# Kernel tuning notes

Measured on AMD Instinct MI355X. Metric: run time of the kernel, lower is better.

## Reference

```python
import jax, jax.numpy as jnp
import numpy as np

BLOCKS = (1, 2, 3, 4)      # (block_size, offset=0) from max_block_size=4
BLOCK_MULT = 12            # lcm(1,2,3,4)
DS = 4                     # downsample_factor
MAX_BS = 4                 # max block size (also pos_conv kernel size)
DIM = 512
VOCAB = 256


def _masked_mean(t, m, axis):
    # t: [..., L, D], m: [..., L] bool -> mean over axis with mask, 0 where empty
    mf = m[..., None].astype(t.dtype)
    num = jnp.sum(t * mf, axis=axis)
    tot = jnp.sum(mf, axis=axis)
    mean = num / jnp.clip(tot, 1.0)
    return jnp.where(tot == 0.0, jnp.zeros_like(mean), mean)


def setup_inputs() -> dict:
    key = jax.random.key(0)
    ks = jax.random.split(key, 8)
    B, S = 8, 2048
    return {
        "x": jax.random.randint(ks[0], (B, S), 0, VOCAB),
        "mask": jnp.ones((B, S), dtype=bool),
        "emb": jax.random.normal(ks[1], (VOCAB, DIM), jnp.float32) * 0.02,
        "dw_w": jax.random.normal(ks[2], (MAX_BS, 1, DIM), jnp.float32) * 0.1,   # depthwise kernel (W, I=1, O=DIM)
        "dw_b": jnp.zeros((DIM,), jnp.float32),
        "pw_w": jax.random.normal(ks[3], (1, DIM, DIM), jnp.float32) * 0.03,     # pointwise 1x1 conv
        "pw_b": jnp.zeros((DIM,), jnp.float32),
        "score_w": jax.random.normal(ks[4], (DIM, 1), jnp.float32) * 0.05,
        "score_b": jnp.zeros((1,), jnp.float32),
    }


def reference(x, mask, emb, dw_w, dw_b, pw_w, pw_b, score_w, score_b):
    B, S = x.shape
    D = DIM
    trunc = ((S + DS - 1) // DS) * DS  # next_divisible_length(S, DS); equals S here

    h = emb[x]                                              # [B,S,D]
    h = jnp.pad(h, ((0, 0), (0, MAX_BS - 1), (0, 0)))       # right pad for VALID conv
    dn = jax.lax.conv_dimension_numbers(h.shape, dw_w.shape, ('NWC', 'WIO', 'NWC'))
    h = jax.lax.conv_general_dilated(h, dw_w, (1,), 'VALID',
                                     dimension_numbers=dn,
                                     feature_group_count=D) + dw_b  # depthwise -> [B,S,D]
    h = jnp.einsum('bsd,de->bse', h, pw_w[0]) + pw_b                # pointwise

    # pad seq to multiple of lcm of block sizes
    Sp = ((h.shape[1] + BLOCK_MULT - 1) // BLOCK_MULT) * BLOCK_MULT
    pad = Sp - h.shape[1]
    h = jnp.pad(h, ((0, 0), (0, pad), (0, 0)))
    m = jnp.pad(mask.astype(bool), ((0, 0), (0, pad)), constant_values=False)

    reprs, rmasks = [], []
    for bsz in BLOCKS:  # fixed small set of block sizes (offset=0 for all)
        nb = Sp // bsz
        g = h.reshape(B, nb, bsz, D)
        mg = m.reshape(B, nb, bsz)
        r = _masked_mean(g, mg, axis=2)                       # [B,nb,D]
        reprs.append(jnp.repeat(r, bsz, axis=1))              # [B,Sp,D]
        rmasks.append(jnp.repeat(jnp.any(mg, axis=-1), bsz, axis=1))

    block_reprs = jnp.stack(reprs, axis=2)    # [B,Sp,M,D]
    block_masks = jnp.stack(rmasks, axis=2)   # [B,Sp,M]

    scores = (block_reprs @ score_w)[..., 0] + score_b[0]     # [B,Sp,M]
    max_neg = -jnp.finfo(scores.dtype).max
    scores = jnp.where(block_masks, scores, max_neg)
    scores = jnp.nan_to_num(jax.nn.softmax(scores, axis=2), nan=0.0)

    # consensus attention over positions
    sim = jnp.einsum('bim,bjm->bij', scores, scores)          # [B,Sp,Sp]
    cm = m[:, :, None] & m[:, None, :]
    sim = jnp.where(cm, sim, max_neg)
    attn = jnp.nan_to_num(jax.nn.softmax(sim, axis=-1), nan=0.0)
    scores = jnp.einsum('bij,bjm->bim', attn, scores)

    out = jnp.einsum('bsmd,bsm->bsd', block_reprs, scores)    # weighted combine
    out = out[:, :trunc]
    mt = m[:, :trunc]

    nl = trunc // DS
    xb = out.reshape(B, nl, DS, D)
    mb = mt.reshape(B, nl, DS)
    out = _masked_mean(xb, mb, axis=2)                        # [B, S/DS, D]
    out_mask = jnp.any(mb, axis=-1)
    return out, out_mask
```

## Files before the change

### kernel.cpp

```cpp
#include <hip/hip_runtime.h>
#include <stdint.h>
#include <stddef.h>

typedef __bf16 bf16_t;
typedef bf16_t bf16x4v __attribute__((ext_vector_type(4)));
typedef bf16_t bf16x8v __attribute__((ext_vector_type(8)));
typedef float  f32x4   __attribute__((ext_vector_type(4)));

#define NBATCH 8
#define SEQ    2048
#define DIM    512
#define SP     2052
#define NB2    1026
#define NB3    684
#define NB4    513
#define NL     512

static __device__ __forceinline__ f32x4 ldbf4(const bf16_t* p) {
  bf16x4v v = *(const bf16x4v*)p;
  f32x4 r;
  r.x = (float)v[0]; r.y = (float)v[1]; r.z = (float)v[2]; r.w = (float)v[3];
  return r;
}
static __device__ __forceinline__ void stbf4(bf16_t* p, f32x4 v) {
  bf16x4v o;
  o[0] = (bf16_t)v.x; o[1] = (bf16_t)v.y; o[2] = (bf16_t)v.z; o[3] = (bf16_t)v.w;
  *(bf16x4v*)p = o;
}

static __device__ __forceinline__ void gload_lds16(const void* g, void* l) {
  __builtin_amdgcn_global_load_lds(
      (const __attribute__((address_space(1))) void*)g,
      (__attribute__((address_space(3))) void*)l, 16, 0, 0);
}

#define GP_WT   256
#define GP_MASK 65
#define GP_AP   512
#define GP_B2   2
__global__ __launch_bounds__(256) void kPrep(
    const float* __restrict__ pw, bf16_t* __restrict__ Wt,
    const void* __restrict__ mraw, float* __restrict__ mask01,
    const float* __restrict__ emb, const float* __restrict__ dww,
    const float* __restrict__ dwb, const float* __restrict__ pwb,
    bf16_t* __restrict__ Ap, float* __restrict__ bias2) {
  const int bx = blockIdx.x, t = threadIdx.x;
  if (bx < GP_WT) {
    __shared__ float T[32][33];
    int ti = bx >> 4, tj = bx & 15;
    int r = t >> 3, c0 = (t & 7) * 4;
    f32x4 v = *(const f32x4*)(pw + (size_t)(ti * 32 + r) * DIM + tj * 32 + c0);
    T[c0 + 0][r] = v.x; T[c0 + 1][r] = v.y;
    T[c0 + 2][r] = v.z; T[c0 + 3][r] = v.w;
    __syncthreads();
    bf16x4v o;
    o[0] = (bf16_t)T[r][c0 + 0]; o[1] = (bf16_t)T[r][c0 + 1];
    o[2] = (bf16_t)T[r][c0 + 2]; o[3] = (bf16_t)T[r][c0 + 3];
    *(bf16x4v*)(Wt + (size_t)(tj * 32 + r) * DIM + ti * 32 + c0) = o;
    return;
  }
  if (bx < GP_WT + GP_MASK) {
    int idx = (bx - GP_WT) * 256 + t;
    if (idx >= NBATCH * SP) return;
    int b = idx / SP, s = idx - b * SP;
    const unsigned char* mb = (const unsigned char*)mraw;
    int u8 = 0;
#pragma unroll
    for (int i = 0; i < 64; i++)
      if ((i & 3) != 0 && mb[i] != 0) u8 = 1;
    float v = 0.f;
    if (s < SEQ) {
      int mi = b * SEQ + s;
      int nz = u8 ? (mb[mi] != 0) : (((const int*)mraw)[mi] != 0);
      v = nz ? 1.f : 0.f;
    }
    mask01[idx] = v;
    return;
  }
  if (bx < GP_WT + GP_MASK + GP_AP) {
    int rp = bx - (GP_WT + GP_MASK);
    int row = rp * 2 + (t >> 7);
    int v = row & 255, tt = row >> 8;
    int d0 = (t & 127) * 4;
    f32x4 e = *(const f32x4*)(emb + (size_t)v * DIM + d0);
    f32x4 w = *(const f32x4*)(dww + tt * DIM + d0);
    stbf4(Ap + (size_t)row * DIM + d0, e * w);
    return;
  }
  {
    int e = (bx - (GP_WT + GP_MASK + GP_AP)) * 256 + t;
    float acc = pwb[e];
#pragma unroll 8
    for (int d = 0; d < DIM; d++) acc += dwb[d] * pw[(size_t)d * DIM + e];
    bias2[e] = acc;
  }
}

#define BM 64
#define BN 128
#define BK 32
__global__ __launch_bounds__(256) void kG_gemm(
    const bf16_t* __restrict__ A, const bf16_t* __restrict__ Bt,
    bf16_t* __restrict__ G) {
  __shared__ __align__(16) bf16_t As[BM * BK];
  __shared__ __align__(16) bf16_t Bs[BN * BK];
  const int t = threadIdx.x;
  const int mt = blockIdx.x >> 2, nt = blockIdx.x & 3;
  const int m0 = mt * BM, n0 = nt * BN;
  const int lane = t & 63, wave = t >> 6;
  const int wm = (wave & 1) * 32, wn = (wave >> 1) * 64;
  const int mloc = lane & 15, quad = lane >> 4;

  f32x4 acc[2][4] = {};

  char* asd  = (char*)As + t * 16;
  char* bsd1 = (char*)Bs + t * 16;
  char* bsd2 = (char*)Bs + (t + 256) * 16;
  const int ar = t >> 2, ak = (t & 3) * 8;
  const int br2 = (t + 256) >> 2;

  for (int k0 = 0; k0 < 512; k0 += BK) {
    gload_lds16(A + (size_t)(m0 + ar) * DIM + k0 + ak, asd);
    gload_lds16(Bt + (size_t)(n0 + ar) * DIM + k0 + ak, bsd1);
    gload_lds16(Bt + (size_t)(n0 + br2) * DIM + k0 + ak, bsd2);
    __syncthreads();
    bf16x8v af[2], bfr[4];
#pragma unroll
    for (int i = 0; i < 2; i++)
      af[i] = *(const bf16x8v*)&As[(wm + i * 16 + mloc) * BK + quad * 8];
#pragma unroll
    for (int i = 0; i < 4; i++)
      bfr[i] = *(const bf16x8v*)&Bs[(wn + i * 16 + mloc) * BK + quad * 8];
#pragma unroll
    for (int mi = 0; mi < 2; mi++)
#pragma unroll
      for (int ni = 0; ni < 4; ni++)
        acc[mi][ni] = __builtin_amdgcn_mfma_f32_16x16x32_bf16(
            af[mi], bfr[ni], acc[mi][ni], 0, 0, 0);
    __syncthreads();
  }
#pragma unroll
  for (int ni = 0; ni < 4; ni++) {
    int col = n0 + wn + ni * 16 + mloc;
#pragma unroll
    for (int mi = 0; mi < 2; mi++) {
      int rbase = m0 + wm + mi * 16 + quad * 4;
#pragma unroll
      for (int r = 0; r < 4; r++)
        G[(size_t)(rbase + r) * DIM + col] = (bf16_t)acc[mi][ni][r];
    }
  }
}

__global__ __launch_bounds__(128) void kBH_levels(
    const int* __restrict__ x, const bf16_t* __restrict__ G,
    const float* __restrict__ bias2, const float* __restrict__ mask01,
    const float* __restrict__ sw, const float* __restrict__ sbp,
    bf16_t* __restrict__ R2, bf16_t* __restrict__ R3, bf16_t* __restrict__ R4,
    float* __restrict__ P) {
  const int b = blockIdx.x, c = blockIdx.y;
  const int s0 = c * 12;
  const int t = threadIdx.x;
  const int d0 = t * 4;
  const float sb = sbp[0];
  __shared__ int xs[15];
  if (t < 15) {
    int sidx = s0 + t;
    xs[t] = (sidx < SEQ) ? x[b * SEQ + sidx] : -1;
  }
  __syncthreads();

  f32x4 b2 = *(const f32x4*)(bias2 + d0);
  f32x4 h[12];
  float ms[12], p[12];
  f32x4 swv = *(const f32x4*)(sw + d0);
#pragma unroll
  for (int i = 0; i < 12; i++) {
    int s = s0 + i;
    ms[i] = mask01[b * SP + s];
    if (s < SEQ) {
      f32x4 acc = b2;
#pragma unroll
      for (int tt = 0; tt < 4; tt++) {
        int xv = xs[i + tt];
        if (xv >= 0)
          acc += ldbf4(G + (size_t)(xv + 256 * tt) * DIM + d0);
      }
      h[i] = acc;
    } else {
      h[i].x = h[i].y = h[i].z = h[i].w = 0.f;
    }
    p[i] = h[i].x * swv.x + h[i].y * swv.y + h[i].z * swv.z + h[i].w * swv.w;
  }
#pragma unroll
  for (int j = 0; j < 6; j++) {
    int i0 = 2 * j;
    float cc = ms[i0] + ms[i0 + 1];
    f32x4 sm = h[i0] * ms[i0] + h[i0 + 1] * ms[i0 + 1];
    float sc = cc > 0.f ? 1.f / cc : 0.f;
    stbf4(R2 + ((size_t)b * NB2 + (c * 6 + j)) * DIM + d0, sm * sc);
  }
#pragma unroll
  for (int j = 0; j < 4; j++) {
    int i0 = 3 * j;
    float cc = ms[i0] + ms[i0 + 1] + ms[i0 + 2];
    f32x4 sm = h[i0] * ms[i0] + h[i0 + 1] * ms[i0 + 1] + h[i0 + 2] * ms[i0 + 2];
    float sc = cc > 0.f ? 1.f / cc : 0.f;
    stbf4(R3 + ((size_t)b * NB3 + (c * 4 + j)) * DIM + d0, sm * sc);
  }
#pragma unroll
  for (int j = 0; j < 3; j++) {
    int i0 = 4 * j;
    float cc = ms[i0] + ms[i0 + 1] + ms[i0 + 2] + ms[i0 + 3];
    f32x4 sm = h[i0] * ms[i0] + h[i0 + 1] * ms[i0 + 1] +
               h[i0 + 2] * ms[i0 + 2] + h[i0 + 3] * ms[i0 + 3];
    float sc = cc > 0.f ? 1.f / cc : 0.f;
    stbf4(R4 + ((size_t)b * NB4 + (c * 3 + j)) * DIM + d0, sm * sc);
  }
#pragma unroll
  for (int off = 32; off > 0; off >>= 1)
#pragma unroll
    for (int i = 0; i < 12; i++) p[i] += __shfl_down(p[i], off);
  __shared__ float hsw[2][12];
  int lane = t & 63, wv = t >> 6;
  if (lane == 0)
#pragma unroll
    for (int i = 0; i < 12; i++) hsw[wv][i] = p[i];
  __syncthreads();
#define HSUM(i) (hsw[0][i] + hsw[1][i])
  if (t < 12) {
    int i = t;
    float m1 = ms[i];
    float v1 = HSUM(i) * m1 + sb;
    int i2 = i & ~1;
    float cc2 = ms[i2] + ms[i2 + 1];
    float s2 = HSUM(i2) * ms[i2] + HSUM(i2 + 1) * ms[i2 + 1];
    float v2 = (cc2 > 0.f ? s2 / cc2 : 0.f) + sb;
    int i3 = (i >= 9) ? 9 : (i >= 6) ? 6 : (i >= 3) ? 3 : 0;
    float cc3 = ms[i3] + ms[i3 + 1] + ms[i3 + 2];
    float s3 = HSUM(i3) * ms[i3] + HSUM(i3 + 1) * ms[i3 + 1] +
               HSUM(i3 + 2) * ms[i3 + 2];
    float v3 = (cc3 > 0.f ? s3 / cc3 : 0.f) + sb;
    int i4 = i & ~3;
    float cc4 = ms[i4] + ms[i4 + 1] + ms[i4 + 2] + ms[i4 + 3];
    float s4 = HSUM(i4) * ms[i4] + HSUM(i4 + 1) * ms[i4 + 1] +
               HSUM(i4 + 2) * ms[i4 + 2] + HSUM(i4 + 3) * ms[i4 + 3];
    float v4 = (cc4 > 0.f ? s4 / cc4 : 0.f) + sb;
    const float NEG = -3.0e38f;
    float a1 = m1 > 0.f ? v1 : NEG, a2 = cc2 > 0.f ? v2 : NEG;
    float a3 = cc3 > 0.f ? v3 : NEG, a4 = cc4 > 0.f ? v4 : NEG;
    float mx = fmaxf(fmaxf(a1, a2), fmaxf(a3, a4));
    f32x4 o;
    if (mx <= NEG) {
      o.x = o.y = o.z = o.w = 0.25f;
    } else {
      float e1 = m1 > 0.f ? __expf(v1 - mx) : 0.f;
      float e2 = cc2 > 0.f ? __expf(v2 - mx) : 0.f;
      float e3 = cc3 > 0.f ? __expf(v3 - mx) : 0.f;
      float e4 = cc4 > 0.f ? __expf(v4 - mx) : 0.f;
      float inv = 1.f / (e1 + e2 + e3 + e4);
      o.x = e1 * inv; o.y = e2 * inv; o.z = e3 * inv; o.w = e4 * inv;
    }
    *(f32x4*)(P + ((size_t)b * SP + s0 + i) * 4) = o;
  }
#undef HSUM
}

#define LQ 2304
__global__ __launch_bounds__(256) void k56_attn_out(
    const float* __restrict__ P, const float* __restrict__ mask01,
    const int* __restrict__ x, const bf16_t* __restrict__ G,
    const float* __restrict__ bias2, const bf16_t* __restrict__ R2,
    const bf16_t* __restrict__ R3, const bf16_t* __restrict__ R4,
    float* __restrict__ out, float* __restrict__ omask) {
  __shared__ f32x4 Qs[LQ];
  __shared__ f32x4 ws4[16];
  __shared__ float msk[16];
  __shared__ float c4w[4];
  __shared__ int xs[20];
  const int b = blockIdx.x, lbase = blockIdx.y * 4;
  const int t = threadIdx.x;
  const int w = t >> 6, lane = t & 63;
  const int smin = lbase * 4;

  if (t < 20) {
    int sidx = smin + t;
    xs[t] = (sidx < SEQ) ? x[b * SEQ + sidx] : -1;
  }
  float cnt0 = 0.f;
#pragma unroll
  for (int it = 0; it < LQ / 256; it++) {
    int j = it * 256 + t;
    f32x4 q; q.x = q.y = q.z = q.w = 0.f;
    if (j < SP) {
      float mf = mask01[b * SP + j];
      if (mf != 0.f) {
        q = *(const f32x4*)(P + ((size_t)b * SP + j) * 4);
      } else {
        cnt0 += 1.f;
      }
    } else {
      cnt0 += 1.f;
    }
    Qs[j] = q;
  }
#pragma unroll
  for (int off = 32; off > 0; off >>= 1) cnt0 += __shfl_down(cnt0, off);
  if (lane == 0) c4w[w] = cnt0;
  __syncthreads();
  const float nmv = c4w[0] + c4w[1] + c4w[2] + c4w[3];

#pragma unroll 1
  for (int k = 0; k < 4; k++) {
    int sl = w * 4 + k;
    int s = smin + sl;
    f32x4 qi = Qs[s];
    f32x4 ac0, ac1, ac2, ac3;
    ac0.x=ac0.y=ac0.z=ac0.w=0.f; ac1=ac0; ac2=ac0; ac3=ac0;
    float dn0 = 0.f, dn1 = 0.f, dn2 = 0.f, dn3 = 0.f;
#pragma unroll 1
    for (int it = 0; it < LQ / 256; it++) {
      int jb = it * 256 + lane;
      f32x4 p0 = Qs[jb], p1 = Qs[jb + 64], p2 = Qs[jb + 128], p3 = Qs[jb + 192];
      float e0 = __expf(qi.x*p0.x + qi.y*p0.y + qi.z*p0.z + qi.w*p0.w);
      float e1 = __expf(qi.x*p1.x + qi.y*p1.y + qi.z*p1.z + qi.w*p1.w);
      float e2 = __expf(qi.x*p2.x + qi.y*p2.y + qi.z*p2.z + qi.w*p2.w);
      float e3 = __expf(qi.x*p3.x + qi.y*p3.y + qi.z*p3.z + qi.w*p3.w);
      dn0 += e0; ac0 += e0 * p0;
      dn1 += e1; ac1 += e1 * p1;
      dn2 += e2; ac2 += e2 * p2;
      dn3 += e3; ac3 += e3 * p3;
    }
    f32x4 acc = (ac0 + ac1) + (ac2 + ac3);
    float den = (dn0 + dn1) + (dn2 + dn3);
#pragma unroll
    for (int off = 32; off > 0; off >>= 1) {
      acc.x += __shfl_down(acc.x, off);
      acc.y += __shfl_down(acc.y, off);
      acc.z += __shfl_down(acc.z, off);
      acc.w += __shfl_down(acc.w, off);
      den   += __shfl_down(den, off);
    }
    if (lane == 0) {
      den -= nmv;
      float inv = den > 0.f ? 1.f / den : 0.f;
      f32x4 wv4; wv4.x = acc.x * inv; wv4.y = acc.y * inv;
      wv4.z = acc.z * inv; wv4.w = acc.w * inv;
      ws4[sl] = wv4;
      msk[sl] = mask01[b * SP + s];
    }
  }
  __syncthreads();

  const int d0 = (t & 127) * 4;
  const f32x4 b2 = *(const f32x4*)(bias2 + d0);
#pragma unroll 1
  for (int p = 0; p < 2; p++) {
    int ll = p * 2 + (t >> 7);
    int l = lbase + ll;
    f32x4 o; o.x = o.y = o.z = o.w = 0.f;
    float cnt = 0.f;
#pragma unroll
    for (int si = 0; si < 4; si++) {
      int sl = ll * 4 + si;
      int s = l * 4 + si;
      float m = msk[sl];
      f32x4 wv4 = ws4[sl];
      f32x4 r1 = b2;
#pragma unroll
      for (int tt = 0; tt < 4; tt++) {
        int xv = xs[sl + tt];
        if (xv >= 0)
          r1 += ldbf4(G + (size_t)(xv + 256 * tt) * DIM + d0);
      }
      f32x4 r2 = ldbf4(R2 + ((size_t)b * NB2 + (s >> 1)) * DIM + d0);
      f32x4 r3 = ldbf4(R3 + ((size_t)b * NB3 + (s / 3)) * DIM + d0);
      f32x4 r4 = ldbf4(R4 + ((size_t)b * NB4 + (s >> 2)) * DIM + d0);
      o += m * (wv4.x * r1 + wv4.y * r2 + wv4.z * r3 + wv4.w * r4);
      cnt += m;
    }
    float inv = cnt > 0.f ? 1.f / cnt : 0.f;
    o *= inv;
    *(f32x4*)(out + ((size_t)b * NL + l) * DIM + d0) = o;
    if ((t & 127) == 0) omask[b * NL + l] = cnt > 0.f ? 1.f : 0.f;
  }
}

extern "C" void kernel_launch(void* const* d_in, const int* in_sizes, int n_in,
                              void* d_out, int out_size, void* d_ws, size_t ws_size,
                              hipStream_t stream) {
  const int*   x    = (const int*)d_in[0];
  const void*  mraw = d_in[1];
  const float* emb  = (const float*)d_in[2];
  const float* dww  = (const float*)d_in[3];
  const float* dwb  = (const float*)d_in[4];
  const float* pw   = (const float*)d_in[5];
  const float* pwb  = (const float*)d_in[6];
  const float* sw   = (const float*)d_in[7];
  const float* sb   = (const float*)d_in[8];

  char* ws = (char*)d_ws;
  size_t off = 0;
  auto alloc = [&](size_t bytes) {
    size_t o = off;
    off = (off + bytes + 255) & ~(size_t)255;
    return o;
  };
  bf16_t* Ap   = (bf16_t*)(ws + alloc((size_t)1024 * DIM * 2));
  bf16_t* G    = (bf16_t*)(ws + alloc((size_t)1024 * DIM * 2));
  bf16_t* Wt   = (bf16_t*)(ws + alloc((size_t)DIM * DIM * 2));
  float* bias2 = (float*)(ws + alloc((size_t)DIM * 4));
  bf16_t* R2   = (bf16_t*)(ws + alloc((size_t)NBATCH * NB2 * DIM * 2));
  bf16_t* R3   = (bf16_t*)(ws + alloc((size_t)NBATCH * NB3 * DIM * 2));
  bf16_t* R4   = (bf16_t*)(ws + alloc((size_t)NBATCH * NB4 * DIM * 2));
  float* mask01 = (float*)(ws + alloc((size_t)NBATCH * SP * 4));
  float* P     = (float*)(ws + alloc((size_t)NBATCH * SP * 4 * 4));

  float* out   = (float*)d_out;
  float* omask = out + (size_t)NBATCH * NL * DIM;

  kPrep<<<GP_WT + GP_MASK + GP_AP + GP_B2, 256, 0, stream>>>(
      pw, Wt, mraw, mask01, emb, dww, dwb, pwb, Ap, bias2);
  kG_gemm<<<64, 256, 0, stream>>>(Ap, Wt, G);
  kBH_levels<<<dim3(NBATCH, 171), 128, 0, stream>>>(x, G, bias2, mask01,
                                                    sw, sb, R2, R3, R4, P);
  k56_attn_out<<<dim3(NBATCH, 128), 256, 0, stream>>>(P, mask01, x, G, bias2,
                                                      R2, R3, R4, out, omask);
}
```

Before: 161.4 us.

## Fuse emb*dw prep into GEMM A-load and restructure attention loop with SoA LDS

```diff
diff --git a/kernel.cpp b/kernel.cpp
--- a/kernel.cpp
+++ b/kernel.cpp
@@ -36,14 +36,12 @@
 
 #define GP_WT   256
 #define GP_MASK 65
-#define GP_AP   512
 #define GP_B2   2
 __global__ __launch_bounds__(256) void kPrep(
     const float* __restrict__ pw, bf16_t* __restrict__ Wt,
     const void* __restrict__ mraw, float* __restrict__ mask01,
-    const float* __restrict__ emb, const float* __restrict__ dww,
     const float* __restrict__ dwb, const float* __restrict__ pwb,
-    bf16_t* __restrict__ Ap, float* __restrict__ bias2) {
+    float* __restrict__ bias2) {
   const int bx = blockIdx.x, t = threadIdx.x;
   if (bx < GP_WT) {
     __shared__ float T[32][33];
@@ -77,18 +75,8 @@
     mask01[idx] = v;
     return;
   }
-  if (bx < GP_WT + GP_MASK + GP_AP) {
-    int rp = bx - (GP_WT + GP_MASK);
-    int row = rp * 2 + (t >> 7);
-    int v = row & 255, tt = row >> 8;
-    int d0 = (t & 127) * 4;
-    f32x4 e = *(const f32x4*)(emb + (size_t)v * DIM + d0);
-    f32x4 w = *(const f32x4*)(dww + tt * DIM + d0);
-    stbf4(Ap + (size_t)row * DIM + d0, e * w);
-    return;
-  }
   {
-    int e = (bx - (GP_WT + GP_MASK + GP_AP)) * 256 + t;
+    int e = (bx - (GP_WT + GP_MASK)) * 256 + t;
     float acc = pwb[e];
 #pragma unroll 8
     for (int d = 0; d < DIM; d++) acc += dwb[d] * pw[(size_t)d * DIM + e];
@@ -100,27 +88,39 @@
 #define BN 128
 #define BK 32
 __global__ __launch_bounds__(256) void kG_gemm(
-    const bf16_t* __restrict__ A, const bf16_t* __restrict__ Bt,
-    bf16_t* __restrict__ G) {
+    const float* __restrict__ emb, const float* __restrict__ dww,
+    const bf16_t* __restrict__ Bt, bf16_t* __restrict__ G) {
   __shared__ __align__(16) bf16_t As[BM * BK];
   __shared__ __align__(16) bf16_t Bs[BN * BK];
   const int t = threadIdx.x;
   const int mt = blockIdx.x >> 2, nt = blockIdx.x & 3;
   const int m0 = mt * BM, n0 = nt * BN;
+  const int t_idx = m0 >> 8, v0 = m0 & 255;
   const int lane = t & 63, wave = t >> 6;
   const int wm = (wave & 1) * 32, wn = (wave >> 1) * 64;
   const int mloc = lane & 15, quad = lane >> 4;
 
   f32x4 acc[2][4] = {};
 
-  char* asd  = (char*)As + t * 16;
   char* bsd1 = (char*)Bs + t * 16;
   char* bsd2 = (char*)Bs + (t + 256) * 16;
   const int ar = t >> 2, ak = (t & 3) * 8;
   const int br2 = (t + 256) >> 2;
 
   for (int k0 = 0; k0 < 512; k0 += BK) {
-    gload_lds16(A + (size_t)(m0 + ar) * DIM + k0 + ak, asd);
+    {
+      const float* ep = emb + (size_t)(v0 + ar) * DIM + k0 + ak;
+      const float* wp = dww + (size_t)t_idx * DIM + k0 + ak;
+      f32x4 e0 = *(const f32x4*)ep, e1 = *(const f32x4*)(ep + 4);
+      f32x4 w0 = *(const f32x4*)wp, w1 = *(const f32x4*)(wp + 4);
+      f32x4 p0 = e0 * w0, p1 = e1 * w1;
+      bf16x8v o;
+      o[0] = (bf16_t)p0.x; o[1] = (bf16_t)p0.y;
+      o[2] = (bf16_t)p0.z; o[3] = (bf16_t)p0.w;
+      o[4] = (bf16_t)p1.x; o[5] = (bf16_t)p1.y;
+      o[6] = (bf16_t)p1.z; o[7] = (bf16_t)p1.w;
+      *(bf16x8v*)&As[ar * BK + ak] = o;
+    }
     gload_lds16(Bt + (size_t)(n0 + ar) * DIM + k0 + ak, bsd1);
     gload_lds16(Bt + (size_t)(n0 + br2) * DIM + k0 + ak, bsd2);
     __syncthreads();
@@ -266,14 +266,14 @@
 #undef HSUM
 }
 
-#define LQ 2304
+#define LQ 2112
 __global__ __launch_bounds__(256) void k56_attn_out(
     const float* __restrict__ P, const float* __restrict__ mask01,
     const int* __restrict__ x, const bf16_t* __restrict__ G,
     const float* __restrict__ bias2, const bf16_t* __restrict__ R2,
     const bf16_t* __restrict__ R3, const bf16_t* __restrict__ R4,
     float* __restrict__ out, float* __restrict__ omask) {
-  __shared__ f32x4 Qs[LQ];
+  __shared__ float Qx[LQ], Qy[LQ], Qz[LQ], Qw[LQ];
   __shared__ f32x4 ws4[16];
   __shared__ float msk[16];
   __shared__ float c4w[4];
@@ -289,8 +289,9 @@
   }
   float cnt0 = 0.f;
 #pragma unroll
-  for (int it = 0; it < LQ / 256; it++) {
+  for (int it = 0; it < 9; it++) {
     int j = it * 256 + t;
+    if (j >= LQ) break;
     f32x4 q; q.x = q.y = q.z = q.w = 0.f;
     if (j < SP) {
       float mf = mask01[b * SP + j];
@@ -302,7 +303,7 @@
     } else {
       cnt0 += 1.f;
     }
-    Qs[j] = q;
+    Qx[j] = q.x; Qy[j] = q.y; Qz[j] = q.z; Qw[j] = q.w;
   }
 #pragma unroll
   for (int off = 32; off > 0; off >>= 1) cnt0 += __shfl_down(cnt0, off);
@@ -310,44 +311,57 @@
   __syncthreads();
   const float nmv = c4w[0] + c4w[1] + c4w[2] + c4w[3];
 
-#pragma unroll 1
-  for (int k = 0; k < 4; k++) {
-    int sl = w * 4 + k;
-    int s = smin + sl;
-    f32x4 qi = Qs[s];
+  {
+    int s0q = smin + w * 4;
+    f32x4 q0, q1, q2, q3;
+    q0.x = Qx[s0q + 0]; q0.y = Qy[s0q + 0]; q0.z = Qz[s0q + 0]; q0.w = Qw[s0q + 0];
+    q1.x = Qx[s0q + 1]; q1.y = Qy[s0q + 1]; q1.z = Qz[s0q + 1]; q1.w = Qw[s0q + 1];
+    q2.x = Qx[s0q + 2]; q2.y = Qy[s0q + 2]; q2.z = Qz[s0q + 2]; q2.w = Qw[s0q + 2];
+    q3.x = Qx[s0q + 3]; q3.y = Qy[s0q + 3]; q3.z = Qz[s0q + 3]; q3.w = Qw[s0q + 3];
     f32x4 ac0, ac1, ac2, ac3;
-    ac0.x=ac0.y=ac0.z=ac0.w=0.f; ac1=ac0; ac2=ac0; ac3=ac0;
+    ac0.x = ac0.y = ac0.z = ac0.w = 0.f; ac1 = ac0; ac2 = ac0; ac3 = ac0;
     float dn0 = 0.f, dn1 = 0.f, dn2 = 0.f, dn3 = 0.f;
 #pragma unroll 1
-    for (int it = 0; it < LQ / 256; it++) {
-      int jb = it * 256 + lane;
-      f32x4 p0 = Qs[jb], p1 = Qs[jb + 64], p2 = Qs[jb + 128], p3 = Qs[jb + 192];
-      float e0 = __expf(qi.x*p0.x + qi.y*p0.y + qi.z*p0.z + qi.w*p0.w);
-      float e1 = __expf(qi.x*p1.x + qi.y*p1.y + qi.z*p1.z + qi.w*p1.w);
-      float e2 = __expf(qi.x*p2.x + qi.y*p2.y + qi.z*p2.z + qi.w*p2.w);
-      float e3 = __expf(qi.x*p3.x + qi.y*p3.y + qi.z*p3.z + qi.w*p3.w);
-      dn0 += e0; ac0 += e0 * p0;
-      dn1 += e1; ac1 += e1 * p1;
-      dn2 += e2; ac2 += e2 * p2;
-      dn3 += e3; ac3 += e3 * p3;
-    }
-    f32x4 acc = (ac0 + ac1) + (ac2 + ac3);
-    float den = (dn0 + dn1) + (dn2 + dn3);
+    for (int it = 0; it < LQ / 64; it++) {
+      int jb = it * 64 + lane;
+      float px = Qx[jb], py = Qy[jb], pz = Qz[jb], pw4 = Qw[jb];
+      float e0 = __expf(q0.x * px + q0.y * py + q0.z * pz + q0.w * pw4);
+      float e1 = __expf(q1.x * px + q1.y * py + q1.z * pz + q1.w * pw4);
+      float e2 = __expf(q2.x * px + q2.y * py + q2.z * pz + q2.w * pw4);
+      float e3 = __expf(q3.x * px + q3.y * py + q3.z * pz + q3.w * pw4);
+      dn0 += e0; ac0.x += e0 * px; ac0.y += e0 * py; ac0.z += e0 * pz; ac0.w += e0 * pw4;
+      dn1 += e1; ac1.x += e1 * px; ac1.y += e1 * py; ac1.z += e1 * pz; ac1.w += e1 * pw4;
+      dn2 += e2; ac2.x += e2 * px; ac2.y += e2 * py; ac2.z += e2 * pz; ac2.w += e2 * pw4;
+      dn3 += e3; ac3.x += e3 * px; ac3.y += e3 * py; ac3.z += e3 * pz; ac3.w += e3 * pw4;
+    }
 #pragma unroll
     for (int off = 32; off > 0; off >>= 1) {
-      acc.x += __shfl_down(acc.x, off);
-      acc.y += __shfl_down(acc.y, off);
-      acc.z += __shfl_down(acc.z, off);
-      acc.w += __shfl_down(acc.w, off);
-      den   += __shfl_down(den, off);
+      ac0.x += __shfl_down(ac0.x, off); ac0.y += __shfl_down(ac0.y, off);
+      ac0.z += __shfl_down(ac0.z, off); ac0.w += __shfl_down(ac0.w, off);
+      dn0 += __shfl_down(dn0, off);
+      ac1.x += __shfl_down(ac1.x, off); ac1.y += __shfl_down(ac1.y, off);
+      ac1.z += __shfl_down(ac1.z, off); ac1.w += __shfl_down(ac1.w, off);
+      dn1 += __shfl_down(dn1, off);
+      ac2.x += __shfl_down(ac2.x, off); ac2.y += __shfl_down(ac2.y, off);
+      ac2.z += __shfl_down(ac2.z, off); ac2.w += __shfl_down(ac2.w, off);
+      dn2 += __shfl_down(dn2, off);
+      ac3.x += __shfl_down(ac3.x, off); ac3.y += __shfl_down(ac3.y, off);
+      ac3.z += __shfl_down(ac3.z, off); ac3.w += __shfl_down(ac3.w, off);
+      dn3 += __shfl_down(dn3, off);
     }
     if (lane == 0) {
-      den -= nmv;
-      float inv = den > 0.f ? 1.f / den : 0.f;
-      f32x4 wv4; wv4.x = acc.x * inv; wv4.y = acc.y * inv;
-      wv4.z = acc.z * inv; wv4.w = acc.w * inv;
-      ws4[sl] = wv4;
-      msk[sl] = mask01[b * SP + s];
+#pragma unroll
+      for (int k = 0; k < 4; k++) {
+        f32x4 acc = (k == 0) ? ac0 : (k == 1) ? ac1 : (k == 2) ? ac2 : ac3;
+        float den = (k == 0) ? dn0 : (k == 1) ? dn1 : (k == 2) ? dn2 : dn3;
+        den -= nmv;
+        float inv = den > 0.f ? 1.f / den : 0.f;
+        f32x4 wv4; wv4.x = acc.x * inv; wv4.y = acc.y * inv;
+        wv4.z = acc.z * inv; wv4.w = acc.w * inv;
+        int sl = w * 4 + k;
+        ws4[sl] = wv4;
+        msk[sl] = mask01[b * SP + smin + sl];
+      }
     }
   }
   __syncthreads();
@@ -406,7 +420,6 @@
     off = (off + bytes + 255) & ~(size_t)255;
     return o;
   };
-  bf16_t* Ap   = (bf16_t*)(ws + alloc((size_t)1024 * DIM * 2));
   bf16_t* G    = (bf16_t*)(ws + alloc((size_t)1024 * DIM * 2));
   bf16_t* Wt   = (bf16_t*)(ws + alloc((size_t)DIM * DIM * 2));
   float* bias2 = (float*)(ws + alloc((size_t)DIM * 4));
@@ -419,9 +432,9 @@
   float* out   = (float*)d_out;
   float* omask = out + (size_t)NBATCH * NL * DIM;
 
-  kPrep<<<GP_WT + GP_MASK + GP_AP + GP_B2, 256, 0, stream>>>(
-      pw, Wt, mraw, mask01, emb, dww, dwb, pwb, Ap, bias2);
-  kG_gemm<<<64, 256, 0, stream>>>(Ap, Wt, G);
+  kPrep<<<GP_WT + GP_MASK + GP_B2, 256, 0, stream>>>(
+      pw, Wt, mraw, mask01, dwb, pwb, bias2);
+  kG_gemm<<<64, 256, 0, stream>>>(emb, dww, Wt, G);
   kBH_levels<<<dim3(NBATCH, 171), 128, 0, stream>>>(x, G, bias2, mask01,
                                                     sw, sb, R2, R3, R4, P);
   k56_attn_out<<<dim3(NBATCH, 128), 256, 0, stream>>>(P, mask01, x, G, bias2,
```

After: 165.6 us. 1.03x slower.
